# Optimization experiments

Measured on AMD Instinct MI355X. Metric: run time of the kernel, lower is better.

## Reference

```python
import jax, jax.numpy as jnp
import numpy as np

N = 100000   # nodes of ntype 'gene'
E = 800000   # edges per metapath
D = 256      # input_dim == output_dim
H = 4        # attn heads
C = D // H   # out_channels per head
M = 2        # num metapaths (tail relations = M + 1, last = self)


def _lrelu(x):
    return jnp.where(x >= 0, x, 0.2 * x)


def _segment_softmax(logits, seg, num_segments):
    # logits: [E, H], seg: [E] int targets
    mx = jax.ops.segment_max(logits, seg, num_segments=num_segments)
    mx = jnp.where(jnp.isfinite(mx), mx, 0.0)  # empty segments -> 0
    ex = jnp.exp(logits - mx[seg])
    den = jax.ops.segment_sum(ex, seg, num_segments=num_segments)
    return ex / (den[seg] + 1e-16)


def setup_inputs() -> dict:
    key = jax.random.key(0)
    ks = jax.random.split(key, 10)
    s = 1.0 / np.sqrt(D)
    return {
        "x": jax.random.normal(ks[0], (N, D), dtype=jnp.float32),
        "edge_index0": jax.random.randint(ks[1], (2, E), 0, N, dtype=jnp.int32),
        "edge_index1": jax.random.randint(ks[2], (2, E), 0, N, dtype=jnp.int32),
        "W_l": jax.random.normal(ks[3], (D, D), dtype=jnp.float32) * s,
        "b_l": jnp.zeros((D,), dtype=jnp.float32),
        "W_r": jax.random.normal(ks[4], (D, D), dtype=jnp.float32) * s,
        "b_r": jnp.zeros((D,), dtype=jnp.float32),
        "attn": jax.random.normal(ks[5], (M, H, 2 * C), dtype=jnp.float32) * (1.0 / np.sqrt(2 * C)),
        "rel_attn_l": jax.random.normal(ks[6], (H, C), dtype=jnp.float32) * (1.0 / np.sqrt(C)),
        "rel_attn_r": jax.random.normal(ks[7], (H, C), dtype=jnp.float32) * (1.0 / np.sqrt(C)),
    }


def reference(x, edge_index0, edge_index1, W_l, b_l, W_r, b_r, attn, rel_attn_l, rel_attn_r):
    # projections -> [N, H, C]  (eval mode: dropout/batchnorm off)
    l = (x @ W_l.T + b_l).reshape(N, H, C)
    r = (x @ W_r.T + b_r).reshape(N, H, C)

    # attn split: first C for x_i (target, r-proj), last C for x_j (source, l-proj);
    # leaky_relu is elementwise so the concat+dot separates exactly.
    def agg(edge_index, m_idx):
        src, tgt = edge_index[0], edge_index[1]
        a_i = jnp.einsum('ehc,hc->eh', _lrelu(r[tgt]), attn[m_idx, :, :C])
        a_j = jnp.einsum('ehc,hc->eh', _lrelu(l[src]), attn[m_idx, :, C:])
        alpha = _segment_softmax(a_i + a_j, tgt, N)          # [E, H]
        msg = l[src] * alpha[:, :, None]                      # [E, H, C]
        return jax.ops.segment_sum(msg, tgt, num_segments=N)  # [N, H, C]

    out0 = agg(edge_index0, 0)
    out1 = agg(edge_index1, 1)
    emb = jnp.stack([out0, out1, r], axis=1)                  # [N, M+1, H, C]

    # relation-level beta attention (get_beta_weights)
    alpha_l = jnp.einsum('nhc,hc->nh', r, rel_attn_l)         # [N, H]
    alpha_r = jnp.einsum('nrhc,hc->nrh', emb, rel_attn_r)     # [N, M+1, H]
    beta = jax.nn.softmax(_lrelu(alpha_l[:, None, :] + alpha_r), axis=1)

    h = (emb * beta[..., None]).sum(axis=1).reshape(N, D)
    return jax.nn.relu(h)
```

## Files before the change

kernel.cpp:

```cpp
#include <hip/hip_runtime.h>
#include <hip/hip_bf16.h>
#include <math.h>

#define D_ 256
#define H_ 4
#define C_ 64

typedef __attribute__((ext_vector_type(8))) short short8;
typedef __attribute__((ext_vector_type(4))) float f32x4;

__device__ inline float lrelu(float v) { return v >= 0.f ? v : 0.2f * v; }

__device__ inline unsigned short f2b(float f) {
    unsigned u = __float_as_uint(f);
    u = (u + 0x7FFFu + ((u >> 16) & 1u)) >> 16;
    return (unsigned short)u;
}
__device__ inline float b2f(unsigned short u) {
    return __uint_as_float(((unsigned)u) << 16);
}

#define GLDS(src, dst) __builtin_amdgcn_global_load_lds(                      \
    (const __attribute__((address_space(1))) void*)(src),                     \
    (__attribute__((address_space(3))) void*)(dst), 16, 0, 0)

__global__ __launch_bounds__(256) void convert_w(
    const float* __restrict__ Wl, const float* __restrict__ Wr,
    unsigned short* __restrict__ Wb)
{
    int i4 = blockIdx.x * 256 + threadIdx.x;
    float4 v = (i4 < 16384) ? ((const float4*)Wl)[i4]
                            : ((const float4*)Wr)[i4 - 16384];
    ushort4 u;
    u.x = f2b(v.x); u.y = f2b(v.y); u.z = f2b(v.z); u.w = f2b(v.w);
    ((ushort4*)Wb)[i4] = u;
}

__device__ __forceinline__ void stage_a(const float* __restrict__ x, float* dst,
                                        int bm, int k0, int wv, int lane, int Mrows)
{
#pragma unroll
    for (int p = 0; p < 4; p++) {
        int ci = (p * 4 + wv) * 64 + lane;
        int row = ci >> 3, cc = ci & 7;
        int gr = bm + row; if (gr >= Mrows) gr = Mrows - 1;
        const float* src = x + (size_t)gr * 256 + k0 + ((cc ^ (row & 7)) << 2);
        GLDS(src, (char*)dst + (size_t)(p * 4 + wv) * 1024);
    }
}
__device__ __forceinline__ void stage_b2(const unsigned short* __restrict__ Wb,
                                         unsigned short* dst, int bn, int k0,
                                         int wv, int lane)
{
#pragma unroll
    for (int p = 0; p < 4; p++) {
        int ci = (p * 4 + wv) * 64 + lane;
        int selb = ci >> 9, cj = ci & 511;
        int col = cj >> 2, cc = cj & 3;
        const unsigned short* src = Wb + (size_t)selb * 65536 +
                                    (size_t)(bn + col) * 256 + k0 +
                                    ((cc ^ ((col >> 1) & 3)) << 3);
        GLDS(src, (char*)dst + (size_t)(p * 4 + wv) * 1024);
    }
}

template <bool RB16>
__global__ __launch_bounds__(256, 2) void gemm_hist(
    const float* __restrict__ x, const unsigned short* __restrict__ Wb,
    const float* __restrict__ b_l, const float* __restrict__ b_r,
    const float* __restrict__ attn, const float* __restrict__ rel_l,
    const float* __restrict__ rel_r,
    unsigned short* __restrict__ lout, void* __restrict__ rout,
    float2* __restrict__ ej2, float* __restrict__ al, float* __restrict__ rd,
    const int* __restrict__ ei0, const int* __restrict__ ei1,
    int* __restrict__ hist,
    int Mrows, int nblkPad, int E_)
{
    const int tid = threadIdx.x;

    if ((int)blockIdx.x >= nblkPad) {
        int e = ((int)blockIdx.x - nblkPad) * 256 + tid;
        if (e < E_) {
            atomicAdd(&hist[ei0[E_ + e]], 1);
            atomicAdd(&hist[Mrows + ei1[E_ + e]], 1);
        }
        return;
    }

    int hw = blockIdx.x;
    int cpx = nblkPad >> 3;
    int orig = (hw & 7) * cpx + (hw >> 3);
    int rt = orig >> 1;
    if (rt * 128 >= Mrows) return;
    const int bn = (orig & 1) * 128;
    const int bm = rt * 128;

    __shared__ float As[2][128 * 32];
    __shared__ unsigned short Bs[2][2][128 * 32];
    const int lane = tid & 63, wv = tid >> 6;
    const int wr = wv >> 1, wc = wv & 1;

    f32x4 accL[4][4], accR[4][4];
#pragma unroll
    for (int m = 0; m < 4; m++)
#pragma unroll
        for (int n = 0; n < 4; n++) { accL[m][n] = (f32x4)0.f; accR[m][n] = (f32x4)0.f; }

    stage_a(x, As[0], bm, 0, wv, lane, Mrows);
    stage_b2(Wb, &Bs[0][0][0], bn, 0, wv, lane);
    __syncthreads();

    int cur = 0;
#pragma unroll
    for (int t = 0; t < 8; t++) {
        if (t < 7) {
            stage_a(x, As[cur ^ 1], bm, (t + 1) * 32, wv, lane, Mrows);
            stage_b2(Wb, &Bs[cur ^ 1][0][0], bn, (t + 1) * 32, wv, lane);
        }
        short8 bfrL[4], bfrR[4], afr[4];
#pragma unroll
        for (int n = 0; n < 4; n++) {
            int col = wc * 64 + n * 16 + (lane & 15);
            int sc = (lane >> 4) ^ ((col >> 1) & 3);
            bfrL[n] = *(const short8*)&Bs[cur][0][col * 32 + sc * 8];
            bfrR[n] = *(const short8*)&Bs[cur][1][col * 32 + sc * 8];
        }
#pragma unroll
        for (int m = 0; m < 4; m++) {
            int row = wr * 64 + m * 16 + (lane & 15);
            int c0 = (lane >> 4) * 2;
            const float* ap = &As[cur][row * 32];
            float4 f0 = *(const float4*)&ap[(c0 ^ (row & 7)) << 2];
            float4 f1 = *(const float4*)&ap[((c0 + 1) ^ (row & 7)) << 2];
            union { short8 v; __hip_bfloat162 b2[4]; } u;
            u.b2[0] = __float22bfloat162_rn(make_float2(f0.x, f0.y));
            u.b2[1] = __float22bfloat162_rn(make_float2(f0.z, f0.w));
            u.b2[2] = __float22bfloat162_rn(make_float2(f1.x, f1.y));
            u.b2[3] = __float22bfloat162_rn(make_float2(f1.z, f1.w));
            afr[m] = u.v;
        }
#pragma unroll
        for (int m = 0; m < 4; m++)
#pragma unroll
            for (int n = 0; n < 4; n++) {
                accL[m][n] = __builtin_amdgcn_mfma_f32_16x16x32_bf16(
                    afr[m], bfrL[n], accL[m][n], 0, 0, 0);
                accR[m][n] = __builtin_amdgcn_mfma_f32_16x16x32_bf16(
                    afr[m], bfrR[n], accR[m][n], 0, 0, 0);
            }
        __syncthreads();
        cur ^= 1;
    }

    const int NH = Mrows * H_;
    const int h = (bn >> 6) + wc;
    float bvl[4], bvr[4], w0[4], w1[4], w2[4], u0[4];
    int gcol[4];
#pragma unroll
    for (int n = 0; n < 4; n++) {
        int c = n * 16 + (lane & 15);
        gcol[n] = bn + wc * 64 + c;
        bvl[n] = b_l[gcol[n]];
        bvr[n] = b_r[gcol[n]];
        w0[n] = attn[(0 * H_ + h) * 128 + 64 + c];
        w1[n] = attn[(1 * H_ + h) * 128 + 64 + c];
        w2[n] = rel_r[h * C_ + c];
        u0[n] = rel_l[h * C_ + c];
    }
#pragma unroll
    for (int m = 0; m < 4; m++) {
#pragma unroll
        for (int q = 0; q < 4; q++) {
            int grow = bm + wr * 64 + m * 16 + (lane >> 4) * 4 + q;
            bool ok = grow < Mrows;
            float p0 = 0.f, p1 = 0.f, p2 = 0.f, q0 = 0.f, q1 = 0.f;
#pragma unroll
            for (int n = 0; n < 4; n++) {
                float vl = accL[m][n][q] + bvl[n];
                float vr = accR[m][n][q] + bvr[n];
                if (ok) {
                    lout[(size_t)grow * 256 + gcol[n]] = f2b(vl);
                    if (RB16) ((unsigned short*)rout)[(size_t)grow * 256 + gcol[n]] = f2b(vr);
                    else      ((float*)rout)[(size_t)grow * 256 + gcol[n]] = vr;
                }
                float lr = lrelu(vl);
                p0 = fmaf(lr, w0[n], p0);
                p1 = fmaf(lr, w1[n], p1);
                p2 = fmaf(vl, w2[n], p2);
                q0 = fmaf(vr, u0[n], q0);
                q1 = fmaf(vr, w2[n], q1);
            }
#pragma unroll
            for (int off = 1; off < 16; off <<= 1) {
                p0 += __shfl_xor(p0, off);
                p1 += __shfl_xor(p1, off);
                p2 += __shfl_xor(p2, off);
                q0 += __shfl_xor(q0, off);
                q1 += __shfl_xor(q1, off);
            }
            if (ok && (lane & 15) == 0) {
                int nh = grow * H_ + h;
                float e0 = __expf(p0), e1 = __expf(p1);
                ej2[nh]      = make_float2(e0, e0 * p2);
                ej2[NH + nh] = make_float2(e1, e1 * p2);
                al[nh] = q0;
                rd[nh] = q1;
            }
        }
    }
}

__global__ __launch_bounds__(256) void scan_a(
    const int* __restrict__ hist, int* __restrict__ segoff,
    int* __restrict__ bsum, int Nn)
{
    int m = blockIdx.y;
    int gid = blockIdx.x * 256 + threadIdx.x;
    int lane = threadIdx.x & 63, wid = threadIdx.x >> 6;
    int v = (gid < Nn) ? hist[m * Nn + gid] : 0;
    int incl = v;
#pragma unroll
    for (int off = 1; off < 64; off <<= 1) {
        int u = __shfl_up(incl, off);
        if (lane >= off) incl += u;
    }
    __shared__ int ws[4], wo[4];
    if (lane == 63) ws[wid] = incl;
    __syncthreads();
    if (threadIdx.x == 0) {
        int run = 0;
#pragma unroll
        for (int i = 0; i < 4; i++) { wo[i] = run; run += ws[i]; }
        bsum[m * 512 + blockIdx.x] = run;
    }
    __syncthreads();
    if (gid < Nn) segoff[m * Nn + gid] = incl - v + wo[wid];
}

__global__ __launch_bounds__(512) void scan_b(int* __restrict__ bsum, int nb)
{
    int m = blockIdx.x;
    int* b = bsum + m * 512;
    int tid = threadIdx.x, lane = tid & 63, wid = tid >> 6;
    int v = (tid < nb) ? b[tid] : 0;
    int incl = v;
#pragma unroll
    for (int off = 1; off < 64; off <<= 1) {
        int u = __shfl_up(incl, off);
        if (lane >= off) incl += u;
    }
    __shared__ int ws[8], wo[8];
    if (lane == 63) ws[wid] = incl;
    __syncthreads();
    if (tid == 0) {
        int run = 0;
#pragma unroll
        for (int i = 0; i < 8; i++) { wo[i] = run; run += ws[i]; }
    }
    __syncthreads();
    if (tid < nb) b[tid] = incl - v + wo[wid];
}

__global__ __launch_bounds__(256) void edge_scatter(
    const int* __restrict__ ei0, const int* __restrict__ ei1,
    const int* __restrict__ segoff, const int* __restrict__ bsum,
    int* __restrict__ cursor, int* __restrict__ srcs, int E_, int Nn)
{
    int e = blockIdx.x * 256 + threadIdx.x;
    if (e >= E_) return;
    int t0 = ei0[E_ + e];
    int p0 = segoff[t0] + bsum[t0 >> 8] + atomicAdd(&cursor[t0], 1);
    srcs[p0] = ei0[e];
    int t1 = ei1[E_ + e];
    int p1 = segoff[Nn + t1] + bsum[512 + (t1 >> 8)] + atomicAdd(&cursor[Nn + t1], 1);
    srcs[E_ + p1] = ei1[e];
}

template <bool RB16>
__global__ __launch_bounds__(256) void aggregate(
    const int* __restrict__ hist, const int* __restrict__ segoff,
    const int* __restrict__ bsum,
    const int* __restrict__ srcs, const float2* __restrict__ ej2,
    const float* __restrict__ al, const float* __restrict__ rd,
    const void* __restrict__ rv, const unsigned short* __restrict__ l,
    float* __restrict__ out, int Nn, int E_)
{
    int lane = threadIdx.x & 63;
    int t = blockIdx.x * 4 + (threadIdx.x >> 6);
    if (t >= Nn) return;
    int h = lane >> 4;
    int NH = Nn * H_;
    int nh = t * H_ + h;

    float4 rrow;
    if (RB16) {
        ushort4 ru = ((const ushort4*)rv)[(size_t)t * 64 + lane];
        rrow = make_float4(b2f(ru.x), b2f(ru.y), b2f(ru.z), b2f(ru.w));
    } else {
        rrow = ((const float4*)rv)[(size_t)t * 64 + lane];
    }
    float a = al[nh];
    float rdv = rd[nh];

    float4 accm[2];
    float denm[2], pnm[2];
#pragma unroll
    for (int m = 0; m < 2; m++) {
        const int* sp = srcs + (size_t)m * E_;
        const float2* ep = ej2 + (size_t)m * NH;
        int beg = segoff[m * Nn + t] + bsum[m * 512 + (t >> 8)];
        int deg = hist[m * Nn + t];

        float4 aA = make_float4(0.f, 0.f, 0.f, 0.f);
        float4 aB = make_float4(0.f, 0.f, 0.f, 0.f);
        float dA = 0.f, dB = 0.f, pA = 0.f, pB = 0.f;
        int j = 0;
#pragma unroll 2
        for (; j + 1 < deg; j += 2) {
            int s0 = sp[beg + j];
            int s1 = sp[beg + j + 1];
            float2 v0 = ep[(size_t)s0 * H_ + h];
            float2 v1 = ep[(size_t)s1 * H_ + h];
            ushort4 l0 = *(const ushort4*)&l[(size_t)s0 * D_ + lane * 4];
            ushort4 l1 = *(const ushort4*)&l[(size_t)s1 * D_ + lane * 4];
            dA += v0.x; pA += v0.y;
            dB += v1.x; pB += v1.y;
            aA.x = fmaf(b2f(l0.x), v0.x, aA.x);
            aA.y = fmaf(b2f(l0.y), v0.x, aA.y);
            aA.z = fmaf(b2f(l0.z), v0.x, aA.z);
            aA.w = fmaf(b2f(l0.w), v0.x, aA.w);
            aB.x = fmaf(b2f(l1.x), v1.x, aB.x);
            aB.y = fmaf(b2f(l1.y), v1.x, aB.y);
            aB.z = fmaf(b2f(l1.z), v1.x, aB.z);
            aB.w = fmaf(b2f(l1.w), v1.x, aB.w);
        }
        if (j < deg) {
            int s0 = sp[beg + j];
            float2 v0 = ep[(size_t)s0 * H_ + h];
            ushort4 l0 = *(const ushort4*)&l[(size_t)s0 * D_ + lane * 4];
            dA += v0.x; pA += v0.y;
            aA.x = fmaf(b2f(l0.x), v0.x, aA.x);
            aA.y = fmaf(b2f(l0.y), v0.x, aA.y);
            aA.z = fmaf(b2f(l0.z), v0.x, aA.z);
            aA.w = fmaf(b2f(l0.w), v0.x, aA.w);
        }
        accm[m] = make_float4(aA.x + aB.x, aA.y + aB.y, aA.z + aB.z, aA.w + aB.w);
        denm[m] = dA + dB;
        pnm[m] = pA + pB;
    }

    float b0 = lrelu(a + pnm[0] / (denm[0] + 1e-16f));
    float b1 = lrelu(a + pnm[1] / (denm[1] + 1e-16f));
    float b2 = lrelu(a + rdv);
    float mm = fmaxf(b0, fmaxf(b1, b2));
    float e0 = __expf(b0 - mm), e1 = __expf(b1 - mm), e2 = __expf(b2 - mm);
    float inv = 1.f / (e0 + e1 + e2);
    float wm0 = e0 * inv / (denm[0] + 1e-16f);
    float wm1 = e1 * inv / (denm[1] + 1e-16f);
    float b2v = e2 * inv;

    float4 o;
    o.x = fmaxf(fmaf(wm0, accm[0].x, fmaf(wm1, accm[1].x, b2v * rrow.x)), 0.f);
    o.y = fmaxf(fmaf(wm0, accm[0].y, fmaf(wm1, accm[1].y, b2v * rrow.y)), 0.f);
    o.z = fmaxf(fmaf(wm0, accm[0].z, fmaf(wm1, accm[1].z, b2v * rrow.z)), 0.f);
    o.w = fmaxf(fmaf(wm0, accm[0].w, fmaf(wm1, accm[1].w, b2v * rrow.w)), 0.f);
    *(float4*)&out[(size_t)t * D_ + lane * 4] = o;
}

extern "C" void kernel_launch(void* const* d_in, const int* in_sizes, int n_in,
                              void* d_out, int out_size, void* d_ws, size_t ws_size,
                              hipStream_t stream) {
    const float* x     = (const float*)d_in[0];
    const int*   ei0   = (const int*)d_in[1];
    const int*   ei1   = (const int*)d_in[2];
    const float* W_l   = (const float*)d_in[3];
    const float* b_l   = (const float*)d_in[4];
    const float* W_r   = (const float*)d_in[5];
    const float* b_r   = (const float*)d_in[6];
    const float* attn  = (const float*)d_in[7];
    const float* rel_l = (const float*)d_in[8];
    const float* rel_r = (const float*)d_in[9];
    float* out = (float*)d_out;

    const int Nn = in_sizes[0] / D_;
    const int E_ = in_sizes[1] / 2;
    const size_t ND = (size_t)Nn * D_;
    const int NH = Nn * H_;

    char* base = (char*)d_ws;
    unsigned short* l = (unsigned short*)base;      size_t off = ND * 2;
    float2* ej2  = (float2*)(base + off); off += (size_t)2 * NH * 8;
    float* al    = (float*)(base + off);  off += (size_t)NH * 4;
    float* rd    = (float*)(base + off);  off += (size_t)NH * 4;
    int* hist    = (int*)(base + off);    off += (size_t)2 * Nn * 4;
    int* cursor  = (int*)(base + off);    off += (size_t)2 * Nn * 4;
    int* segoff  = (int*)(base + off);    off += (size_t)2 * Nn * 4;
    int* bsum    = (int*)(base + off);    off += (size_t)1024 * 4;
    int* srcs    = (int*)(base + off);    off += (size_t)2 * E_ * 4;
    unsigned short* Wb = (unsigned short*)(base + off); off += (size_t)2 * 65536 * 2;
    unsigned short* rb = (unsigned short*)(base + off);
    const bool rb16 = (ws_size >= off + ND * 2);
    void* r_any = rb16 ? (void*)rb : (void*)out;

    hipMemsetAsync(hist, 0, (size_t)4 * Nn * 4, stream);

    convert_w<<<128, 256, 0, stream>>>(W_l, W_r, Wb);

    int rowTiles = (Nn + 127) / 128;
    int nblk = 2 * rowTiles;
    int nblkPad = (nblk + 7) & ~7;
    int eb = (E_ + 255) / 256;
    if (rb16)
        gemm_hist<true ><<<nblkPad + eb, 256, 0, stream>>>(
            x, Wb, b_l, b_r, attn, rel_l, rel_r, l, r_any, ej2, al, rd,
            ei0, ei1, hist, Nn, nblkPad, E_);
    else
        gemm_hist<false><<<nblkPad + eb, 256, 0, stream>>>(
            x, Wb, b_l, b_r, attn, rel_l, rel_r, l, r_any, ej2, al, rd,
            ei0, ei1, hist, Nn, nblkPad, E_);

    int nb = (Nn + 255) / 256;
    scan_a<<<dim3(nb, 2), 256, 0, stream>>>(hist, segoff, bsum, Nn);
    scan_b<<<2, 512, 0, stream>>>(bsum, nb);
    edge_scatter<<<eb, 256, 0, stream>>>(ei0, ei1, segoff, bsum, cursor, srcs, E_, Nn);

    if (rb16)
        aggregate<true ><<<(Nn + 3) / 4, 256, 0, stream>>>(
            hist, segoff, bsum, srcs, ej2, al, rd, r_any, l, out, Nn, E_);
    else
        aggregate<false><<<(Nn + 3) / 4, 256, 0, stream>>>(
            hist, segoff, bsum, srcs, ej2, al, rd, r_any, l, out, Nn, E_);
}
```

Measured before the change: 395.7 us.

## Load GEMM MFMA fragments directly from global memory, dropping LDS staging

Removes the double-buffered LDS staging (global_load_lds with swizzle) for the x and bf16 weight tiles in the fused projection GEMM. Each lane now loads its MFMA A and B fragments straight from global memory, and the per-step barriers go away. This saves LDS capacity and synchronisation, which may allow more occupancy. The cost is that data is no longer shared across waves: each wave re-reads the same x rows and weight columns from cache, and there is no explicit prefetch to overlap loads with compute.

```diff
diff --git a/kernel.cpp b/kernel.cpp
--- a/kernel.cpp
+++ b/kernel.cpp
@@ -19,10 +19,6 @@
 __device__ inline float b2f(unsigned short u) {
     return __uint_as_float(((unsigned)u) << 16);
 }
-
-#define GLDS(src, dst) __builtin_amdgcn_global_load_lds(                      \
-    (const __attribute__((address_space(1))) void*)(src),                     \
-    (__attribute__((address_space(3))) void*)(dst), 16, 0, 0)
 
 __global__ __launch_bounds__(256) void convert_w(
     const float* __restrict__ Wl, const float* __restrict__ Wr,
@@ -34,34 +30,6 @@
     ushort4 u;
     u.x = f2b(v.x); u.y = f2b(v.y); u.z = f2b(v.z); u.w = f2b(v.w);
     ((ushort4*)Wb)[i4] = u;
-}
-
-__device__ __forceinline__ void stage_a(const float* __restrict__ x, float* dst,
-                                        int bm, int k0, int wv, int lane, int Mrows)
-{
-#pragma unroll
-    for (int p = 0; p < 4; p++) {
-        int ci = (p * 4 + wv) * 64 + lane;
-        int row = ci >> 3, cc = ci & 7;
-        int gr = bm + row; if (gr >= Mrows) gr = Mrows - 1;
-        const float* src = x + (size_t)gr * 256 + k0 + ((cc ^ (row & 7)) << 2);
-        GLDS(src, (char*)dst + (size_t)(p * 4 + wv) * 1024);
-    }
-}
-__device__ __forceinline__ void stage_b2(const unsigned short* __restrict__ Wb,
-                                         unsigned short* dst, int bn, int k0,
-                                         int wv, int lane)
-{
-#pragma unroll
-    for (int p = 0; p < 4; p++) {
-        int ci = (p * 4 + wv) * 64 + lane;
-        int selb = ci >> 9, cj = ci & 511;
-        int col = cj >> 2, cc = cj & 3;
-        const unsigned short* src = Wb + (size_t)selb * 65536 +
-                                    (size_t)(bn + col) * 256 + k0 +
-                                    ((cc ^ ((col >> 1) & 3)) << 3);
-        GLDS(src, (char*)dst + (size_t)(p * 4 + wv) * 1024);
-    }
 }
 
 template <bool RB16>
@@ -95,8 +63,6 @@
     const int bn = (orig & 1) * 128;
     const int bm = rt * 128;
 
-    __shared__ float As[2][128 * 32];
-    __shared__ unsigned short Bs[2][2][128 * 32];
     const int lane = tid & 63, wv = tid >> 6;
     const int wr = wv >> 1, wc = wv & 1;
 
@@ -106,32 +72,34 @@
 #pragma unroll
         for (int n = 0; n < 4; n++) { accL[m][n] = (f32x4)0.f; accR[m][n] = (f32x4)0.f; }
 
-    stage_a(x, As[0], bm, 0, wv, lane, Mrows);
-    stage_b2(Wb, &Bs[0][0][0], bn, 0, wv, lane);
-    __syncthreads();
-
-    int cur = 0;
+    int rowg[4];
+#pragma unroll
+    for (int m = 0; m < 4; m++) {
+        int r = bm + wr * 64 + m * 16 + (lane & 15);
+        rowg[m] = (r < Mrows) ? r : (Mrows - 1);
+    }
+    const int koff = (lane >> 4) * 8;
+    const unsigned short* bbase[4];
+#pragma unroll
+    for (int n = 0; n < 4; n++) {
+        int col = bn + wc * 64 + n * 16 + (lane & 15);
+        bbase[n] = Wb + (size_t)col * 256 + koff;
+    }
+
 #pragma unroll
     for (int t = 0; t < 8; t++) {
-        if (t < 7) {
-            stage_a(x, As[cur ^ 1], bm, (t + 1) * 32, wv, lane, Mrows);
-            stage_b2(Wb, &Bs[cur ^ 1][0][0], bn, (t + 1) * 32, wv, lane);
-        }
+        const int k0 = t * 32;
         short8 bfrL[4], bfrR[4], afr[4];
 #pragma unroll
         for (int n = 0; n < 4; n++) {
-            int col = wc * 64 + n * 16 + (lane & 15);
-            int sc = (lane >> 4) ^ ((col >> 1) & 3);
-            bfrL[n] = *(const short8*)&Bs[cur][0][col * 32 + sc * 8];
-            bfrR[n] = *(const short8*)&Bs[cur][1][col * 32 + sc * 8];
+            bfrL[n] = *(const short8*)(bbase[n] + k0);
+            bfrR[n] = *(const short8*)(bbase[n] + 65536 + k0);
         }
 #pragma unroll
         for (int m = 0; m < 4; m++) {
-            int row = wr * 64 + m * 16 + (lane & 15);
-            int c0 = (lane >> 4) * 2;
-            const float* ap = &As[cur][row * 32];
-            float4 f0 = *(const float4*)&ap[(c0 ^ (row & 7)) << 2];
-            float4 f1 = *(const float4*)&ap[((c0 + 1) ^ (row & 7)) << 2];
+            const float* ap = x + (size_t)rowg[m] * 256 + k0 + koff;
+            float4 f0 = *(const float4*)ap;
+            float4 f1 = *(const float4*)(ap + 4);
             union { short8 v; __hip_bfloat162 b2[4]; } u;
             u.b2[0] = __float22bfloat162_rn(make_float2(f0.x, f0.y));
             u.b2[1] = __float22bfloat162_rn(make_float2(f0.z, f0.w));
@@ -148,8 +116,6 @@
                 accR[m][n] = __builtin_amdgcn_mfma_f32_16x16x32_bf16(
                     afr[m], bfrR[n], accR[m][n], 0, 0, 0);
             }
-        __syncthreads();
-        cur ^= 1;
     }
 
     const int NH = Mrows * H_;
```

Result: slower. 456.9 us (+15.5%).
